# Kernel tuning notes

Hardware: AMD Instinct MI355X
Metric: run time of the kernel (lower is better)

The kernel has to match this reference:

```python
import jax, jax.numpy as jnp
import numpy as np

B, S, V, D, H, KVH, L = 2, 1024, 8192, 1024, 16, 4, 8
HD = D // H          # 64, head dim
KV = KVH * HD        # 256, kv projection width
HID = 2736           # max(16, ceil(2*4*1024/48)*16)
NS = 4               # num_skip_weights = min(L//2, L - L//2)
SOFTCAP = 30.0
ROPE_BASE = 10000.0
RS_INIT = 1.0 / np.sqrt(L)


def setup_inputs() -> dict:
    key = jax.random.key(0)
    ks = iter(jax.random.split(key, 64))
    def rn(shape, s=0.02):
        return jax.random.normal(next(ks), shape, dtype=jnp.float32) * s
    inp = {}
    inp['idx'] = jax.random.randint(next(ks), (B, S), 0, V)
    inp['tok_emb'] = rn((V, D))
    inp['embed_norm_w'] = 1.0 + rn((D,))
    inp['resid_mix'] = jnp.stack([1.0 + rn((L, D), 0.05), rn((L, D), 0.05)], axis=1)  # [L,2,D]
    inp['attn_norm_w'] = 1.0 + rn((L, D))
    inp['mlp_norm_w'] = 1.0 + rn((L, D))
    inp['attn_scale'] = RS_INIT + rn((L, D))
    inp['mlp_scale'] = RS_INIT + rn((L, D))
    inp['Wq'] = rn((L, D, D))
    inp['Wk'] = rn((L, KV, D))
    inp['Wv'] = rn((L, KV, D))
    conv = lambda C: rn((L, 3, C), 0.1).at[:, 2, :].add(1.0)  # curr ~ 1, prev ~ 0
    inp['q_conv_w'] = conv(D)
    inp['k_conv_w'] = conv(KV)
    inp['v_conv_w'] = conv(KV)
    inp['q_gain'] = jnp.eye(H, dtype=jnp.float32)[None] + rn((L, H, H))
    inp['post_attn_norm_w'] = 1.0 + rn((L, D))
    inp['Wo'] = rn((L, D, D))
    inp['Wfc'] = rn((L, HID, D))
    inp['Wgate'] = rn((L, HID, D))
    inp['h_conv_w'] = rn((L, 3, HID), 0.1).at[:, 2, :].add(1.0)
    inp['h_norm_w'] = 1.0 + rn((L, HID))
    inp['Wmproj'] = rn((L, D, HID))
    inp['skip_weights'] = RS_INIT + rn((NS, D))
    inp['skip_gates'] = rn((NS, D), 0.1)
    inp['final_norm_w'] = 1.0 + rn((D,))
    inp['lm_head_w'] = rn((V, D))
    inp['bigram_head'] = rn((V, V))
    inp['bigram_scale'] = 0.02 + rn((V,), 0.005)
    inp['bigram_gate'] = rn((D,), 0.1)
    inp['unigram_bias'] = rn((V,), 0.01)
    return inp


def _rmsnorm(x, w=None):
    eps = jnp.finfo(x.dtype).eps
    y = x * jax.lax.rsqrt(jnp.mean(x * x, axis=-1, keepdims=True) + eps)
    return y * w if w is not None else y


def _dwconv(x, w):  # x [B,S,C], w [3,C]: causal depthwise 3-tap conv
    n = x.shape[1]
    xp = jnp.pad(x, ((0, 0), (2, 0), (0, 0)))
    return w[0] * xp[:, :n] + w[1] * xp[:, 1:n + 1] + w[2] * xp[:, 2:]


def _rope_tables(seqlen):
    inv_freq = 1.0 / (ROPE_BASE ** (jnp.arange(0, HD, 2, dtype=jnp.float32) / HD))
    freqs = jnp.outer(jnp.arange(seqlen, dtype=jnp.float32), inv_freq)  # [S, HD//2]
    return jnp.cos(freqs)[None, None], jnp.sin(freqs)[None, None]


def _apply_rope(x, cos, sin):
    half = x.shape[-1] // 2
    x1, x2 = x[..., :half], x[..., half:]
    return jnp.concatenate([x1 * cos + x2 * sin, -x1 * sin + x2 * cos], axis=-1)


def reference(idx, tok_emb, embed_norm_w, resid_mix, attn_norm_w, mlp_norm_w, attn_scale, mlp_scale, Wq, Wk, Wv, q_conv_w, k_conv_w, v_conv_w, q_gain, post_attn_norm_w, Wo, Wfc, Wgate, h_conv_w, h_norm_w, Wmproj, skip_weights, skip_gates, final_norm_w, lm_head_w, bigram_head, bigram_scale, bigram_gate, unigram_bias):
    cos, sin = _rope_tables(S)
    causal = jnp.tril(jnp.ones((S, S), dtype=bool))

    def attn(x, i):
        q = _dwconv(x @ Wq[i].T, q_conv_w[i]).reshape(B, S, H, HD).transpose(0, 2, 1, 3)
        k = _dwconv(x @ Wk[i].T, k_conv_w[i]).reshape(B, S, KVH, HD).transpose(0, 2, 1, 3)
        v = _dwconv(x @ Wv[i].T, v_conv_w[i]).reshape(B, S, KVH, HD).transpose(0, 2, 1, 3)
        q = _apply_rope(_rmsnorm(q), cos, sin)
        k = _apply_rope(_rmsnorm(k), cos, sin)
        q = jnp.einsum('hg,bgsd->bhsd', q_gain[i], q)
        kr = jnp.repeat(k, H // KVH, axis=1)
        vr = jnp.repeat(v, H // KVH, axis=1)
        scores = jnp.einsum('bhsd,bhtd->bhst', q, kr) / np.sqrt(HD).astype(np.float32)
        scores = jnp.where(causal, scores, -jnp.inf)
        p = jax.nn.softmax(scores, axis=-1)
        y = jnp.einsum('bhst,bhtd->bhsd', p, vr).transpose(0, 2, 1, 3).reshape(B, S, D)
        return _rmsnorm(y, post_attn_norm_w[i]) @ Wo[i].T

    def mlp(x, i):
        h = (x @ Wfc[i].T) * jax.nn.silu(x @ Wgate[i].T)
        h = _rmsnorm(_dwconv(h, h_conv_w[i]), h_norm_w[i])
        return h @ Wmproj[i].T

    def block(x, x0, i):
        x = resid_mix[i, 0] * x + resid_mix[i, 1] * x0
        x = x + attn_scale[i] * attn(_rmsnorm(x, attn_norm_w[i]), i)
        x = x + mlp_scale[i] * mlp(_rmsnorm(x, mlp_norm_w[i]), i)
        return x

    x = _rmsnorm(tok_emb[idx], embed_norm_w)
    x0 = x
    enc = L // 2
    skips = []
    for i in range(enc):
        x = block(x, x0, i)
        skips.append(x)
    for j in range(L - enc):
        if j < NS:
            x = x + (skip_weights[j] * jax.nn.sigmoid(skip_gates[j]))[None, None, :] * skips.pop()
        x = block(x, x0, enc + j)
    x = _rmsnorm(x, final_norm_w)

    logits = x @ lm_head_w.T + unigram_bias
    gate = jax.nn.sigmoid(x @ bigram_gate)[..., None]        # [B,S,1]
    logits = logits + gate * (bigram_head[idx] * bigram_scale)
    return SOFTCAP * jnp.tanh(logits / SOFTCAP)
```

## Files before the change

kernel.cpp:

```cpp
#include <hip/hip_runtime.h>
#include <hip/hip_bf16.h>
#include <cstdint>
#include <cstddef>

#define B_   2
#define S_   1024
#define V_   8192
#define D_   1024
#define H_   16
#define KVH_ 4
#define L_   8
#define HD_  64
#define KV_  256
#define HID_ 2736
#define HIDP 2752
#define NT_  (B_*S_)
#define EPSF 1.1920928955078125e-7f
#define SOFTCAPF 30.0f

typedef __bf16 bf8 __attribute__((ext_vector_type(8)));
typedef __bf16 bf4 __attribute__((ext_vector_type(4)));
typedef float  f4  __attribute__((ext_vector_type(4)));

#define GLDS16(g, l) __builtin_amdgcn_global_load_lds( \
    (const __attribute__((address_space(1))) void*)(g), \
    (__attribute__((address_space(3))) void*)(l), 16, 0, 0)

__device__ __forceinline__ float wsum(float v){
#pragma unroll
  for (int m = 32; m >= 1; m >>= 1) v += __shfl_xor(v, m, 64);
  return v;
}
__device__ __forceinline__ float blocksum256(float v){
  __shared__ float red[4];
  v = wsum(v);
  if ((threadIdx.x & 63) == 0) red[threadIdx.x >> 6] = v;
  __syncthreads();
  return red[0] + red[1] + red[2] + red[3];
}
__device__ __forceinline__ float4 ld4b(const __bf16* p, size_t i4){
  bf4 v = ((const bf4*)p)[i4];
  return make_float4((float)v[0], (float)v[1], (float)v[2], (float)v[3]);
}

template<int BM, int BN, int OUT>
__global__ __launch_bounds__(256) void k_gemm(
    const __bf16* __restrict__ A, const __bf16* __restrict__ Wt,
    void* __restrict__ Cv, int M, int N, int K, int lda, int mtiles,
    const int* __restrict__ idx, const float* __restrict__ gateb,
    const float* __restrict__ bhd, const float* __restrict__ bsc,
    const float* __restrict__ ub)
{
  constexpr int SMEM = ((BM + BN) * 128 > 32768 || OUT == 2) ? 32768 : (BM + BN) * 128;
  __shared__ __attribute__((aligned(16))) unsigned char smem[SMEM];
  __bf16* As = (__bf16*)smem;
  __bf16* Bs = (__bf16*)(smem + BM*128);

  const int tid  = threadIdx.x;
  const int nwg = gridDim.x;
  const int wg  = (blockIdx.x & 7) * (nwg >> 3) + (blockIdx.x >> 3);
  const int bm   = wg % mtiles;
  const int bn   = wg / mtiles;
  const int m0   = bm * BM, n0 = bn * BN;
  const int lane = tid & 63, wv = tid >> 6;
  const int wm   = (wv >> 1) * (BM / 2);
  const int wn   = (wv & 1) * (BN / 2);
  const int fr   = lane & 15, g = lane >> 4;
  constexpr int MI = BM / 32;
  constexpr int NJ = BN / 32;
  constexpr int AP = BM / 32;
  constexpr int BP = BN / 32;

  f4 acc[MI][NJ] = {};

  const int rs = lane >> 3, ss = lane & 7;
  const int cseg = ss ^ ((wv*8 + rs) & 7);
  const __bf16* aq[AP];
#pragma unroll
  for (int p = 0; p < AP; ++p)
    aq[p] = A + (size_t)(m0 + wv*8 + p*32 + rs) * lda + cseg*8;
  const __bf16* bq[BP];
#pragma unroll
  for (int p = 0; p < BP; ++p) {
    int rB = n0 + wv*8 + p*32 + rs; if (rB > N-1) rB = N-1;
    bq[p] = Wt + (size_t)rB * K + cseg*8;
  }

  for (int k0 = 0; k0 < K; k0 += 64) {
    __syncthreads();
#pragma unroll
    for (int p = 0; p < AP; ++p) GLDS16(aq[p] + k0, As + (wv*8 + p*32)*64);
#pragma unroll
    for (int p = 0; p < BP; ++p) GLDS16(bq[p] + k0, Bs + (wv*8 + p*32)*64);
    __syncthreads();

#pragma unroll
    for (int ks = 0; ks < 2; ++ks) {
      const int sgo = (((ks*4 + g) ^ (fr & 7)) << 3);
      bf8 af[MI], bf[NJ];
#pragma unroll
      for (int i = 0; i < MI; ++i)
        af[i] = *(const bf8*)&As[(wm + i*16 + fr)*64 + sgo];
#pragma unroll
      for (int j = 0; j < NJ; ++j)
        bf[j] = *(const bf8*)&Bs[(wn + j*16 + fr)*64 + sgo];
#pragma unroll
      for (int i = 0; i < MI; ++i)
#pragma unroll
        for (int j = 0; j < NJ; ++j)
          acc[i][j] = __builtin_amdgcn_mfma_f32_16x16x32_bf16(af[i], bf[j], acc[i][j], 0, 0, 0);
    }
  }

  if constexpr (OUT == 2) {
    float* EP = (float*)smem;
    __syncthreads();
#pragma unroll
    for (int i = 0; i < MI; ++i)
#pragma unroll
      for (int j = 0; j < NJ; ++j)
#pragma unroll
        for (int r = 0; r < 4; ++r)
          EP[(wm + i*16 + g*4 + r)*128 + wn + j*16 + fr] = acc[i][j][r];
    __syncthreads();
#pragma unroll
    for (int it = 0; it < 8; ++it) {
      int row = it*8 + (tid >> 5);
      int c0  = (tid & 31) << 2;
      int grow = m0 + row;
      int gn   = n0 + c0;
      float gt = gateb[grow];
      int   tk = idx[grow];
      float4 a4 = *(float4*)&EP[row*128 + c0];
      float4 b4 = *(const float4*)&bhd[(size_t)tk * V_ + gn];
      float4 u4 = *(const float4*)&ub[gn];
      float4 s4 = *(const float4*)&bsc[gn];
      float4 o;
      o.x = SOFTCAPF * tanhf((a4.x + u4.x + gt*b4.x*s4.x) / SOFTCAPF);
      o.y = SOFTCAPF * tanhf((a4.y + u4.y + gt*b4.y*s4.y) / SOFTCAPF);
      o.z = SOFTCAPF * tanhf((a4.z + u4.z + gt*b4.z*s4.z) / SOFTCAPF);
      o.w = SOFTCAPF * tanhf((a4.w + u4.w + gt*b4.w*s4.w) / SOFTCAPF);
      *(float4*)&((float*)Cv)[(size_t)grow * N + gn] = o;
    }
  } else {
    const int rbase = g << 2;
#pragma unroll
    for (int i = 0; i < MI; ++i) {
      int gm = m0 + wm + i*16 + rbase;
#pragma unroll
      for (int j = 0; j < NJ; ++j) {
        int gn = n0 + wn + j*16 + fr;
        if (gn < N) {
          if constexpr (OUT == 1) {
#pragma unroll
            for (int r = 0; r < 4; ++r)
              ((__bf16*)Cv)[(size_t)(gm + r) * N + gn] = (__bf16)acc[i][j][r];
          } else {
#pragma unroll
            for (int r = 0; r < 4; ++r)
              ((float*)Cv)[(size_t)(gm + r) * N + gn] = acc[i][j][r];
          }
        }
      }
    }
  }
}

__global__ void k_cvt(const float* __restrict__ s, __bf16* __restrict__ d,
                      int perL, int K, int Kpad, long dstL, long dstOff, long nd4)
{
  long i = (long)blockIdx.x * 256 + threadIdx.x;
  if (i >= nd4) return;
  const int kp4 = Kpad >> 2;
  long row = i / kp4;
  int  c   = (int)(i % kp4) << 2;
  long layer = row / perL, r = row % perL;
  bf4 o;
  if (c < K) {
    float4 v = *(const float4*)(s + (layer*perL + r) * (long)K + c);
    o[0] = (__bf16)v.x; o[1] = (__bf16)v.y; o[2] = (__bf16)v.z; o[3] = (__bf16)v.w;
  } else { o[0] = o[1] = o[2] = o[3] = (__bf16)0.f; }
  *(bf4*)(d + layer*dstL + dstOff + (long)r*Kpad + c) = o;
}

__global__ void k_embed(const int* __restrict__ idx, const float* __restrict__ emb,
                        const float* __restrict__ wn, float* __restrict__ x, float* __restrict__ x0)
{
  const int r = blockIdx.x, t = threadIdx.x;
  const float4 v = ((const float4*)(emb + (size_t)idx[r] * D_))[t];
  float ss = blocksum256(v.x*v.x + v.y*v.y + v.z*v.z + v.w*v.w);
  float rs = rsqrtf(ss / (float)D_ + EPSF);
  const float4 w = ((const float4*)wn)[t];
  float4 o = make_float4(v.x*rs*w.x, v.y*rs*w.y, v.z*rs*w.z, v.w*rs*w.w);
  ((float4*)(x  + (size_t)r * D_))[t] = o;
  ((float4*)(x0 + (size_t)r * D_))[t] = o;
}

__global__ void k_blockstart(
    float* __restrict__ x, const float* __restrict__ x0,
    const __bf16* __restrict__ t1, const float* __restrict__ msc,
    float* __restrict__ skstore, const float* __restrict__ skread, int same,
    const float* __restrict__ skw, const float* __restrict__ skg,
    const float* __restrict__ mix, const float* __restrict__ nw,
    __bf16* __restrict__ xn)
{
  const int r = blockIdx.x, t = threadIdx.x;
  const size_t i4 = (size_t)r * 256 + t;
  float4 xv = ((float4*)x)[i4];
  if (t1) {
    float4 tv = ld4b(t1, i4);
    float4 s  = ((const float4*)msc)[t];
    xv.x += s.x*tv.x; xv.y += s.y*tv.y; xv.z += s.z*tv.z; xv.w += s.w*tv.w;
  }
  if (skstore) ((float4*)skstore)[i4] = xv;
  if (skw) {
    float4 sv;
    if (same) sv = xv;
    else      sv = ((const float4*)skread)[i4];
    float4 w = ((const float4*)skw)[t];
// ... 65 lines not shown
  float bb = (s >= 1) ? (float)p0[-ld]   : 0.f;
  return w[c]*a + w[C + c]*bb + w[2*C + c]*(float)p0[0];
}

__global__ __launch_bounds__(256) void k_prep(
    const __bf16* __restrict__ qkv,
    const float* __restrict__ qcw, const float* __restrict__ kcw, const float* __restrict__ vcw,
    const float* __restrict__ qgain,
    __bf16* __restrict__ q2, __bf16* __restrict__ k2, __bf16* __restrict__ v2)
{
  const int tok = blockIdx.x;
  const int s = tok & (S_ - 1);
  const int t = threadIdx.x, lane = t & 63, w = t >> 6;
  __shared__ float qsh[1024];

  const int j = lane & 31;
  float freq = __expf(-(float)j * (9.210340371976184f / 32.f));
  float sn, cs;
  __sincosf((float)s * freq, &sn, &cs);

#pragma unroll
  for (int k = 0; k < 4; ++k) {
    int c = t + k*256;
    float qc = conv3b(qkv, tok, s, 1536, c, qcw, D_, c);
    float ssq = wsum(qc * qc);
    float qn = qc * rsqrtf(ssq / 64.f + EPSF);
    float pr = __shfl_xor(qn, 32, 64);
    qsh[c] = qn * cs + ((lane < 32) ? pr * sn : -pr * sn);
  }
  __syncthreads();
  float qg[16];
#pragma unroll
  for (int g = 0; g < 16; ++g) qg[g] = qsh[g*64 + lane];
#pragma unroll
  for (int k = 0; k < 4; ++k) {
    int h = (k << 2) + w;
    float acc = 0.f;
#pragma unroll
    for (int g = 0; g < 16; ++g) acc += qgain[h*16 + g] * qg[g];
    q2[(size_t)tok * D_ + h*64 + lane] = (__bf16)acc;
  }

  {
    float kc = conv3b(qkv, tok, s, 1536, 1024 + t, kcw, KV_, t);
    float ssk = wsum(kc * kc);
    float kn = kc * rsqrtf(ssk / 64.f + EPSF);
    float pk = __shfl_xor(kn, 32, 64);
    k2[(size_t)tok * KV_ + t] = (__bf16)(kn * cs + ((lane < 32) ? pk * sn : -pk * sn));
  }
  v2[(size_t)tok * KV_ + t] = (__bf16)conv3b(qkv, tok, s, 1536, 1280 + t, vcw, KV_, t);
}

#define LDK 72
__global__ __launch_bounds__(256) void k_attn(
    const __bf16* __restrict__ q2, const __bf16* __restrict__ k2,
    const __bf16* __restrict__ v2, float* __restrict__ y)
{
  __shared__ __attribute__((aligned(16))) __bf16 Ks[64*LDK];
  __shared__ __attribute__((aligned(16))) __bf16 Vt[64*LDK];
  __shared__ __attribute__((aligned(16))) __bf16 Ps[4][16*LDK];

  const int id = blockIdx.x;
  const int qb = id & 15;
  const int h  = (id >> 4) & 15;
  const int b  = id >> 8;
  const int tid = threadIdx.x, l = tid & 63, wq = tid >> 6;
  const int g = l >> 4, fr = l & 15;
  const int kvh = h >> 2;
  const int qrow = qb*64 + wq*16 + fr;

  bf8 qf[2];
#pragma unroll
  for (int ks = 0; ks < 2; ++ks)
    qf[ks] = *(const bf8*)&q2[(size_t)(b*S_ + qrow)*D_ + h*64 + g*8 + ks*32];

  float m = -1e30f, lsum = 0.f;
  f4 acc[4] = {};

  const int nch = qb + 1;
  for (int ch = 0; ch < nch; ++ch) {
    const int t0 = ch << 6;
    __syncthreads();
#pragma unroll
    for (int it = 0; it < 2; ++it) {
      int i = tid + it*256;
      int row = i >> 3, seg = (i & 7) << 3;
      *(bf8*)&Ks[row*LDK + seg] =
        *(const bf8*)&k2[(size_t)(b*S_ + t0 + row)*KV_ + kvh*64 + seg];
    }
    {
      int key4 = (tid & 15) << 2, hd4 = (tid >> 4) << 2;
      bf4 vv[4];
#pragma unroll
      for (int kk = 0; kk < 4; ++kk)
        vv[kk] = *(const bf4*)&v2[(size_t)(b*S_ + t0 + key4 + kk)*KV_ + kvh*64 + hd4];
#pragma unroll
      for (int hh = 0; hh < 4; ++hh) {
        bf4 w = { vv[0][hh], vv[1][hh], vv[2][hh], vv[3][hh] };
        *(bf4*)&Vt[(hd4 + hh)*LDK + key4] = w;
      }
    }
    __syncthreads();

    f4 sc[4] = {};
#pragma unroll
    for (int ks = 0; ks < 2; ++ks)
#pragma unroll
      for (int t = 0; t < 4; ++t) {
        bf8 kf = *(const bf8*)&Ks[(t*16 + fr)*LDK + g*8 + ks*32];
        sc[t] = __builtin_amdgcn_mfma_f32_16x16x32_bf16(kf, qf[ks], sc[t], 0, 0, 0);
      }

    const bool lastch = (ch == qb);
    float s[4][4];
    float pmax = -1e30f;
#pragma unroll
    for (int t = 0; t < 4; ++t)
#pragma unroll
      for (int r = 0; r < 4; ++r) {
        float v = sc[t][r] * 0.125f;
        if (lastch && (t0 + t*16 + g*4 + r > qrow)) v = -1e30f;
        s[t][r] = v;
        pmax = fmaxf(pmax, v);
      }
    pmax = fmaxf(pmax, __shfl_xor(pmax, 16, 64));
    pmax = fmaxf(pmax, __shfl_xor(pmax, 32, 64));
    float mnew = fmaxf(m, pmax);
    float alpha = __expf(m - mnew);
    float rs = 0.f;
#pragma unroll
    for (int t = 0; t < 4; ++t)
#pragma unroll
      for (int r = 0; r < 4; ++r) { float p = __expf(s[t][r] - mnew); s[t][r] = p; rs += p; }
    rs += __shfl_xor(rs, 16, 64);
    rs += __shfl_xor(rs, 32, 64);
    lsum = lsum * alpha + rs;
    m = mnew;
#pragma unroll
    for (int t = 0; t < 4; ++t) acc[t] = acc[t] * alpha;

#pragma unroll
    for (int t = 0; t < 4; ++t) {
      bf4 pw = { (__bf16)s[t][0], (__bf16)s[t][1], (__bf16)s[t][2], (__bf16)s[t][3] };
      *(bf4*)&Ps[wq][fr*LDK + t*16 + g*4] = pw;
    }

#pragma unroll
    for (int ks = 0; ks < 2; ++ks) {
      bf8 pf = *(const bf8*)&Ps[wq][fr*LDK + g*8 + ks*32];
#pragma unroll
      for (int t = 0; t < 4; ++t) {
        bf8 vf = *(const bf8*)&Vt[(t*16 + fr)*LDK + g*8 + ks*32];
        acc[t] = __builtin_amdgcn_mfma_f32_16x16x32_bf16(vf, pf, acc[t], 0, 0, 0);
      }
    }
  }

  float inv = 1.f / lsum;
#pragma unroll
  for (int t = 0; t < 4; ++t)
#pragma unroll
    for (int r = 0; r < 4; ++r)
      y[(size_t)(b*S_ + qrow)*D_ + h*64 + t*16 + g*4 + r] = acc[t][r] * inv;
}

__device__ __forceinline__ float hprodb(const __bf16* row, int c){
  float a = (float)row[c], b = (float)row[HID_ + c];
  return a * b / (1.f + __expf(-b));
}
__global__ __launch_bounds__(256) void k_hfuse(
    const __bf16* __restrict__ hb, const float* __restrict__ cw,
    const float* __restrict__ nw, __bf16* __restrict__ out)
{
  const int tok = blockIdx.x, t = threadIdx.x;
  const int s = tok & (S_ - 1);
  const __bf16* row0 = hb + (size_t)tok * 5472;
  float v[11]; float ss = 0.f;
#pragma unroll
  for (int ii = 0; ii < 11; ++ii) {
    int c = t + ii*256;
    float cv = 0.f;
    if (c < HID_) {
      float p0 = hprodb(row0, c);
      float p1 = (s >= 1) ? hprodb(row0 - 5472, c) : 0.f;
      float p2 = (s >= 2) ? hprodb(row0 - 2*5472, c) : 0.f;
      cv = cw[c]*p2 + cw[HID_ + c]*p1 + cw[2*HID_ + c]*p0;
    }
    v[ii] = cv; ss += cv*cv;
  }
  ss = blocksum256(ss);
  float rs = rsqrtf(ss / (float)HID_ + EPSF);
#pragma unroll
  for (int ii = 0; ii < 11; ++ii) {
    int c = t + ii*256;
    if (c < HIDP)
      out[(size_t)tok * HIDP + c] = (c < HID_) ? (__bf16)(v[ii]*rs*nw[c]) : (__bf16)0.f;
  }
}

template<int BM, int BN, int OUT>
static inline void gemm(const __bf16* A, const __bf16* W, void* C, int M, int N, int K,
                        int lda, hipStream_t s,
                        const int* idx = nullptr, const float* gateb = nullptr,
                        const float* bhd = nullptr, const float* bsc = nullptr,
                        const float* ub = nullptr)
{
  int mt = M / BM, nt = (N + BN - 1) / BN;
  k_gemm<BM, BN, OUT><<<dim3(mt * nt), dim3(256), 0, s>>>(A, W, C, M, N, K, lda, mt,
                                                          idx, gateb, bhd, bsc, ub);
}

extern "C" void kernel_launch(void* const* d_in, const int* in_sizes, int n_in,
                              void* d_out, int out_size, void* d_ws, size_t ws_size,
                              hipStream_t stream)
{
  const int*   idx    = (const int*)d_in[0];
  const float* temb   = (const float*)d_in[1];
  const float* enw    = (const float*)d_in[2];
  const float* rmix   = (const float*)d_in[3];
  const float* anw    = (const float*)d_in[4];
  const float* mnw    = (const float*)d_in[5];
  const float* ascale = (const float*)d_in[6];
  const float* mscale = (const float*)d_in[7];
  const float* Wq     = (const float*)d_in[8];
  const float* Wk     = (const float*)d_in[9];
  const float* Wv     = (const float*)d_in[10];
  const float* qcw    = (const float*)d_in[11];
  const float* kcw    = (const float*)d_in[12];
  const float* vcw    = (const float*)d_in[13];
  const float* qgain  = (const float*)d_in[14];
  const float* panw   = (const float*)d_in[15];
  const float* Wo     = (const float*)d_in[16];
  const float* Wfc    = (const float*)d_in[17];
  const float* Wgate  = (const float*)d_in[18];
  const float* hcw    = (const float*)d_in[19];
  const float* hnw    = (const float*)d_in[20];
  const float* Wmp    = (const float*)d_in[21];
  const float* skw    = (const float*)d_in[22];
  const float* skg    = (const float*)d_in[23];
  const float* fnw    = (const float*)d_in[24];
  const float* lmw    = (const float*)d_in[25];
  const float* bh     = (const float*)d_in[26];
  const float* bsc    = (const float*)d_in[27];
  const float* bg     = (const float*)d_in[28];
  const float* ub     = (const float*)d_in[29];

  float* p = (float*)d_ws;
  float* x    = p; p += (size_t)NT_ * D_;
  float* x0   = p; p += (size_t)NT_ * D_;
  float* y    = p; p += (size_t)NT_ * D_;
  float* skips= p; p += (size_t)4 * NT_ * D_;
  float* gateb= p; p += NT_;
  __bf16* qkvb= (__bf16*)p; p += (size_t)NT_ * 1536 / 2;
  __bf16* hbb = (__bf16*)p; p += (size_t)NT_ * 5472 / 2;
  __bf16* t1b = (__bf16*)p; p += (size_t)NT_ * D_ / 2;
  __bf16* xnb = (__bf16*)p; p += (size_t)NT_ * D_ / 2;
  __bf16* q2b = (__bf16*)p; p += (size_t)NT_ * D_ / 2;
  __bf16* k2b = (__bf16*)p; p += (size_t)NT_ * KV_ / 2;
  __bf16* v2b = (__bf16*)p; p += (size_t)NT_ * KV_ / 2;
  __bf16* hnb = (__bf16*)p; p += (size_t)NT_ * HIDP / 2;
  __bf16* wqkv= (__bf16*)p; p += (size_t)L_ * 1536 * 1024 / 2;
  __bf16* wob = (__bf16*)p; p += (size_t)L_ * 1024 * 1024 / 2;
  __bf16* wfcg= (__bf16*)p; p += (size_t)L_ * 5472 * 1024 / 2;
  __bf16* wmpb= (__bf16*)p; p += (size_t)L_ * 1024 * HIDP / 2;
  __bf16* wlmb= (__bf16*)p; p += (size_t)V_ * 1024 / 2;
  float* logits = (float*)d_out;

  auto cvt = [&](const float* s, __bf16* d, int perL, int K, int Kpad,
                 long dstL, long dstOff, int nl) {
    long nd4 = (long)nl * perL * (Kpad >> 2);
    int grid = (int)((nd4 + 255) / 256);
    k_cvt<<<grid, 256, 0, stream>>>(s, d, perL, K, Kpad, dstL, dstOff, nd4);
  };
  cvt(Wq,    wqkv, 1024, 1024, 1024, 1536L*1024, 0,          L_);
  cvt(Wk,    wqkv,  256, 1024, 1024, 1536L*1024, 1024L*1024, L_);
  cvt(Wv,    wqkv,  256, 1024, 1024, 1536L*1024, 1280L*1024, L_);
  cvt(Wo,    wob,  1024, 1024, 1024, 1024L*1024, 0,          L_);
  cvt(Wfc,   wfcg, 2736, 1024, 1024, 5472L*1024, 0,          L_);
  cvt(Wgate, wfcg, 2736, 1024, 1024, 5472L*1024, 2736L*1024, L_);
  cvt(Wmp,   wmpb, 1024, 2736, HIDP, 1024L*HIDP, 0,          L_);
  cvt(lmw,   wlmb, 8192, 1024, 1024, 8192L*1024, 0,          1);

  k_embed<<<NT_, 256, 0, stream>>>(idx, temb, enw, x, x0);

  for (int i = 0; i < L_; ++i) {
    const float* pmsc = (i > 0) ? mscale + (size_t)(i-1) * D_ : nullptr;
    float* skst = (i >= 1 && i <= 4) ? skips + (size_t)(i-1) * NT_ * D_ : nullptr;
    const float* skrd = (i >= 4) ? skips + (size_t)(7-i) * NT_ * D_ : nullptr;
    const float* swp = (i >= 4) ? skw + (size_t)(i-4) * D_ : nullptr;
    const float* sgp = (i >= 4) ? skg + (size_t)(i-4) * D_ : nullptr;
    k_blockstart<<<NT_, 256, 0, stream>>>(x, x0, (i > 0) ? t1b : nullptr, pmsc,
                                          skst, skrd, (i == 4) ? 1 : 0, swp, sgp,
                                          rmix + (size_t)i * 2 * D_,
                                          anw + (size_t)i * D_, xnb);
    gemm<64, 128, 1>(xnb, wqkv + (size_t)i * 1536 * 1024, qkvb, NT_, 1536, 1024, 1024, stream);
    k_prep<<<NT_, 256, 0, stream>>>(qkvb,
                                    qcw + (size_t)i * 3 * D_, kcw + (size_t)i * 3 * KV_,
                                    vcw + (size_t)i * 3 * KV_, qgain + (size_t)i * H_ * H_,
                                    q2b, k2b, v2b);
    k_attn<<<B_ * H_ * (S_/64), 256, 0, stream>>>(q2b, k2b, v2b, y);
    k_rmsnormb<<<NT_, 256, 0, stream>>>(y, panw + (size_t)i * D_, xnb);
    gemm<64, 64, 1>(xnb, wob + (size_t)i * 1024 * 1024, t1b, NT_, 1024, 1024, 1024, stream);
    k_addnorm<<<NT_, 256, 0, stream>>>(x, t1b, ascale + (size_t)i * D_,
                                       mnw + (size_t)i * D_, xnb, nullptr, nullptr);
    gemm<64, 128, 1>(xnb, wfcg + (size_t)i * 5472 * 1024, hbb, NT_, 5472, 1024, 1024, stream);
    k_hfuse<<<NT_, 256, 0, stream>>>(hbb, hcw + (size_t)i * 3 * HID_,
                                     hnw + (size_t)i * HID_, hnb);
    gemm<64, 64, 1>(hnb, wmpb + (size_t)i * 1024 * HIDP, t1b, NT_, 1024, HIDP, HIDP, stream);
  }

  k_addnorm<<<NT_, 256, 0, stream>>>(x, t1b, mscale + (size_t)7 * D_, fnw, xnb, bg, gateb);
  gemm<64, 128, 2>(xnb, wlmb, logits, NT_, V_, 1024, 1024, stream, idx, gateb, bh, bsc, ub);
}
```

Baseline: 1.920 ms.

## Add 256x256 triple-buffered 8-wave GEMM for MLP up-projection and LM head

Adds a new GEMM kernel with 256x256 tiles, 512 threads (8 waves), three LDS buffers fed by global_load_lds, explicit vmcnt waits and barriers, and setprio around the MFMA bursts. It is used for the large fc/gate projection (N=5472) and the LM head with its fused bigram/softcap epilogue, which now runs in four 64-row passes through LDS. The goal is more operand reuse per loaded byte and overlap of loads with MFMA. The cost is 96KB of LDS per block, which limits occupancy, and wasted work on partial N tiles, since 5472 is not a multiple of 256 and out-of-range B rows are clamped.

New measurement: 1.914 ms. Within noise of the previous version (-0.3%).

```diff
diff --git a/kernel.cpp b/kernel.cpp
--- a/kernel.cpp
+++ b/kernel.cpp
@@ -46,12 +46,9 @@
 template<int BM, int BN, int OUT>
 __global__ __launch_bounds__(256) void k_gemm(
     const __bf16* __restrict__ A, const __bf16* __restrict__ Wt,
-    void* __restrict__ Cv, int M, int N, int K, int lda, int mtiles,
-    const int* __restrict__ idx, const float* __restrict__ gateb,
-    const float* __restrict__ bhd, const float* __restrict__ bsc,
-    const float* __restrict__ ub)
-{
-  constexpr int SMEM = ((BM + BN) * 128 > 32768 || OUT == 2) ? 32768 : (BM + BN) * 128;
+    void* __restrict__ Cv, int M, int N, int K, int lda, int mtiles)
+{
+  constexpr int SMEM = (BM + BN) * 128;
   __shared__ __attribute__((aligned(16))) unsigned char smem[SMEM];
   __bf16* As = (__bf16*)smem;
   __bf16* Bs = (__bf16*)(smem + BM*128);
@@ -112,59 +109,181 @@
     }
   }
 
-  if constexpr (OUT == 2) {
+  const int rbase = g << 2;
+#pragma unroll
+  for (int i = 0; i < MI; ++i) {
+    int gm = m0 + wm + i*16 + rbase;
+#pragma unroll
+    for (int j = 0; j < NJ; ++j) {
+      int gn = n0 + wn + j*16 + fr;
+      if (gn < N) {
+        if constexpr (OUT == 1) {
+#pragma unroll
+          for (int r = 0; r < 4; ++r)
+            ((__bf16*)Cv)[(size_t)(gm + r) * N + gn] = (__bf16)acc[i][j][r];
+        } else {
+#pragma unroll
+          for (int r = 0; r < 4; ++r)
+            ((float*)Cv)[(size_t)(gm + r) * N + gn] = acc[i][j][r];
+        }
+      }
+    }
+  }
+}
+
+#define STG8(t, h, b) do { \
+    if ((h) < 2) { \
+      const __bf16* _s = A + (size_t)(m0 + (h)*128 + w16 + rsub) * lda + (t)*32 + sseg*8; \
+      GLDS16(_s, smem + (b)*32768 + ((h)*128 + w16) * 64); \
+    } else { \
+      int _rB = n0 + ((h)-2)*128 + w16 + rsub; if (_rB > N-1) _rB = N-1; \
+      const __bf16* _s = Wt + (size_t)_rB * K + (t)*32 + sseg*8; \
+      GLDS16(_s, smem + (b)*32768 + 16384 + (((h)-2)*128 + w16) * 64); \
+    } } while (0)
+
+#define LDA8(b, r, gg) (*(const bf8*)(smem + (b)*32768 + (r)*64 + (((gg) ^ ((((r)>>3)&1)<<1)))*16))
+#define LDB8(b, r, gg) (*(const bf8*)(smem + (b)*32768 + 16384 + (r)*64 + (((gg) ^ ((((r)>>3)&1)<<1)))*16))
+
+#define PH8(bt, q, dostage, st, sh, sb, W) do { \
+    const int _r0 = wr*128 + ((q)>>1)*64 + fr; \
+    const int _c0 = wc*64 + ((q)&1)*32 + fr; \
+    bf8 _a0 = LDA8(bt, _r0 +  0, g); \
+    bf8 _a1 = LDA8(bt, _r0 + 16, g); \
+    bf8 _a2 = LDA8(bt, _r0 + 32, g); \
+    bf8 _a3 = LDA8(bt, _r0 + 48, g); \
+    bf8 _b0 = LDB8(bt, _c0 +  0, g); \
+    bf8 _b1 = LDB8(bt, _c0 + 16, g); \
+    if (dostage) STG8(st, sh, sb); \
+    if ((W) == 4)      asm volatile("s_waitcnt vmcnt(4)" ::: "memory"); \
+    else if ((W) == 0) asm volatile("s_waitcnt vmcnt(0)" ::: "memory"); \
+    asm volatile("" ::: "memory"); \
+    __builtin_amdgcn_s_barrier(); \
+    asm volatile("" ::: "memory"); \
+    __builtin_amdgcn_s_setprio(1); \
+    acc[((q)>>1)*4+0][((q)&1)*2+0] = __builtin_amdgcn_mfma_f32_16x16x32_bf16(_a0, _b0, acc[((q)>>1)*4+0][((q)&1)*2+0], 0,0,0); \
+    acc[((q)>>1)*4+0][((q)&1)*2+1] = __builtin_amdgcn_mfma_f32_16x16x32_bf16(_a0, _b1, acc[((q)>>1)*4+0][((q)&1)*2+1], 0,0,0); \
+    acc[((q)>>1)*4+1][((q)&1)*2+0] = __builtin_amdgcn_mfma_f32_16x16x32_bf16(_a1, _b0, acc[((q)>>1)*4+1][((q)&1)*2+0], 0,0,0); \
+    acc[((q)>>1)*4+1][((q)&1)*2+1] = __builtin_amdgcn_mfma_f32_16x16x32_bf16(_a1, _b1, acc[((q)>>1)*4+1][((q)&1)*2+1], 0,0,0); \
+    acc[((q)>>1)*4+2][((q)&1)*2+0] = __builtin_amdgcn_mfma_f32_16x16x32_bf16(_a2, _b0, acc[((q)>>1)*4+2][((q)&1)*2+0], 0,0,0); \
+    acc[((q)>>1)*4+2][((q)&1)*2+1] = __builtin_amdgcn_mfma_f32_16x16x32_bf16(_a2, _b1, acc[((q)>>1)*4+2][((q)&1)*2+1], 0,0,0); \
+    acc[((q)>>1)*4+3][((q)&1)*2+0] = __builtin_amdgcn_mfma_f32_16x16x32_bf16(_a3, _b0, acc[((q)>>1)*4+3][((q)&1)*2+0], 0,0,0); \
+    acc[((q)>>1)*4+3][((q)&1)*2+1] = __builtin_amdgcn_mfma_f32_16x16x32_bf16(_a3, _b1, acc[((q)>>1)*4+3][((q)&1)*2+1], 0,0,0); \
+    __builtin_amdgcn_s_setprio(0); \
+    asm volatile("" ::: "memory"); \
+    __builtin_amdgcn_s_barrier(); \
+    asm volatile("" ::: "memory"); \
+  } while (0)
+
+template<int OUT>
+__global__ __launch_bounds__(512, 2) void k_gemm8(
+    const __bf16* __restrict__ A, const __bf16* __restrict__ Wt,
+    void* __restrict__ Cv, int M, int N, int K, int lda, int mtiles,
+    const int* __restrict__ idx, const float* __restrict__ gateb,
+    const float* __restrict__ bhd, const float* __restrict__ bsc,
+    const float* __restrict__ ub)
+{
+  __shared__ __attribute__((aligned(16))) unsigned char smem[98304];
+  const int tid = threadIdx.x;
+  const int nwg = gridDim.x;
+  const int wg  = (blockIdx.x & 7) * (nwg >> 3) + (blockIdx.x >> 3);
+  const int bm = wg % mtiles, bnn = wg / mtiles;
+  const int m0 = bm << 8, n0 = bnn << 8;
+  const int l = tid & 63, wid = tid >> 6;
+  const int wr = wid >> 2, wc = wid & 3;
+  const int fr = l & 15, g = l >> 4;
+
+  f4 acc[8][4] = {};
+
+  const int w16  = wid * 16;
+  const int rsub = l >> 2;
+  const int sseg = (l & 3) ^ ((l >= 32) ? 2 : 0);
+
+  const int nk = K >> 5;
+  const int ni = nk >> 1;
+
+  STG8(0, 0, 0); STG8(0, 1, 0); STG8(0, 2, 0); STG8(0, 3, 0);
+  STG8(1, 0, 1); STG8(1, 1, 1); STG8(1, 2, 1); STG8(1, 3, 1);
+  asm volatile("s_waitcnt vmcnt(4)" ::: "memory");
+  asm volatile("" ::: "memory");
+  __builtin_amdgcn_s_barrier();
+  asm volatile("" ::: "memory");
+
+  int b0 = 0;
+  for (int i = 0; i < ni; ++i) {
+    const int b1 = (b0 == 2) ? 0 : b0 + 1;
+    const int b2 = (b1 == 2) ? 0 : b1 + 1;
+    const bool nlast = (i + 1 < ni);
+    const int t2 = 2*i + 2, t3 = 2*i + 3;
+    PH8(b0, 0, nlast, t2, 0, b2, -1);
+    PH8(b0, 1, nlast, t2, 1, b2, -1);
+    PH8(b0, 2, nlast, t2, 2, b2, -1);
+    PH8(b0, 3, nlast, t2, 3, b2, nlast ? 4 : 0);
+    PH8(b1, 0, nlast, t3, 0, b0, -1);
+    PH8(b1, 1, nlast, t3, 1, b0, -1);
+    PH8(b1, 2, nlast, t3, 2, b0, -1);
+    PH8(b1, 3, nlast, t3, 3, b0, nlast ? 4 : -1);
+    b0 = b2;
+  }
+
+  if constexpr (OUT == 1) {
+    __bf16* C = (__bf16*)Cv;
+#pragma unroll
+    for (int ii = 0; ii < 8; ++ii) {
+      int gm = m0 + wr*128 + ii*16 + g*4;
+#pragma unroll
+      for (int j = 0; j < 4; ++j) {
+        int gn = n0 + wc*64 + j*16 + fr;
+        if (gn < N) {
+#pragma unroll
+          for (int r = 0; r < 4; ++r)
+            C[(size_t)(gm + r) * N + gn] = (__bf16)acc[ii][j][r];
+        }
+      }
+    }
+  } else {
     float* EP = (float*)smem;
     __syncthreads();
 #pragma unroll
-    for (int i = 0; i < MI; ++i)
-#pragma unroll
-      for (int j = 0; j < NJ; ++j)
-#pragma unroll
-        for (int r = 0; r < 4; ++r)
-          EP[(wm + i*16 + g*4 + r)*128 + wn + j*16 + fr] = acc[i][j][r];
-    __syncthreads();
-#pragma unroll
-    for (int it = 0; it < 8; ++it) {
-      int row = it*8 + (tid >> 5);
-      int c0  = (tid & 31) << 2;
-      int grow = m0 + row;
-      int gn   = n0 + c0;
-      float gt = gateb[grow];
-      int   tk = idx[grow];
-      float4 a4 = *(float4*)&EP[row*128 + c0];
-      float4 b4 = *(const float4*)&bhd[(size_t)tk * V_ + gn];
-      float4 u4 = *(const float4*)&ub[gn];
-      float4 s4 = *(const float4*)&bsc[gn];
-      float4 o;
-      o.x = SOFTCAPF * tanhf((a4.x + u4.x + gt*b4.x*s4.x) / SOFTCAPF);
-      o.y = SOFTCAPF * tanhf((a4.y + u4.y + gt*b4.y*s4.y) / SOFTCAPF);
-      o.z = SOFTCAPF * tanhf((a4.z + u4.z + gt*b4.z*s4.z) / SOFTCAPF);
-      o.w = SOFTCAPF * tanhf((a4.w + u4.w + gt*b4.w*s4.w) / SOFTCAPF);
-      *(float4*)&((float*)Cv)[(size_t)grow * N + gn] = o;
-    }
-  } else {
-    const int rbase = g << 2;
-#pragma unroll
-    for (int i = 0; i < MI; ++i) {
-      int gm = m0 + wm + i*16 + rbase;
-#pragma unroll
-      for (int j = 0; j < NJ; ++j) {
-        int gn = n0 + wn + j*16 + fr;
-        if (gn < N) {
-          if constexpr (OUT == 1) {
+    for (int pass = 0; pass < 4; ++pass) {
+      if (wr == (pass >> 1)) {
+#pragma unroll
+        for (int a = 0; a < 4; ++a) {
+          int ii = (pass & 1)*4 + a;
+#pragma unroll
+          for (int j = 0; j < 4; ++j)
 #pragma unroll
             for (int r = 0; r < 4; ++r)
-              ((__bf16*)Cv)[(size_t)(gm + r) * N + gn] = (__bf16)acc[i][j][r];
-          } else {
-#pragma unroll
-            for (int r = 0; r < 4; ++r)
-              ((float*)Cv)[(size_t)(gm + r) * N + gn] = acc[i][j][r];
-          }
+              EP[(a*16 + g*4 + r)*256 + wc*64 + j*16 + fr] = acc[ii][j][r];
         }
       }
-    }
-  }
-}
+      __syncthreads();
+#pragma unroll
+      for (int it = 0; it < 8; ++it) {
+        int row = it*8 + (tid >> 6);
+        int c0  = (tid & 63) << 2;
+        int grow = m0 + pass*64 + row;
+        int gn = n0 + c0;
+        float gt = gateb[grow];
+        int tk = idx[grow];
+        float4 a4 = *(float4*)&EP[row*256 + c0];
+        float4 b4 = *(const float4*)&bhd[(size_t)tk * V_ + gn];
+        float4 u4 = *(const float4*)&ub[gn];
+        float4 s4 = *(const float4*)&bsc[gn];
+        float4 o;
+        o.x = SOFTCAPF * tanhf((a4.x + u4.x + gt*b4.x*s4.x) / SOFTCAPF);
+        o.y = SOFTCAPF * tanhf((a4.y + u4.y + gt*b4.y*s4.y) / SOFTCAPF);
+        o.z = SOFTCAPF * tanhf((a4.z + u4.z + gt*b4.z*s4.z) / SOFTCAPF);
+        o.w = SOFTCAPF * tanhf((a4.w + u4.w + gt*b4.w*s4.w) / SOFTCAPF);
+        *(float4*)&((float*)Cv)[(size_t)grow * N + gn] = o;
+      }
+      __syncthreads();
+    }
+  }
+}
+#undef PH8
+#undef LDA8
+#undef LDB8
+#undef STG8
 
 __global__ void k_cvt(const float* __restrict__ s, __bf16* __restrict__ d,
                       int perL, int K, int Kpad, long dstL, long dstOff, long nd4)
@@ -484,14 +603,22 @@
 
 template<int BM, int BN, int OUT>
 static inline void gemm(const __bf16* A, const __bf16* W, void* C, int M, int N, int K,
-                        int lda, hipStream_t s,
-                        const int* idx = nullptr, const float* gateb = nullptr,
-                        const float* bhd = nullptr, const float* bsc = nullptr,
-                        const float* ub = nullptr)
+                        int lda, hipStream_t s)
 {
   int mt = M / BM, nt = (N + BN - 1) / BN;
-  k_gemm<BM, BN, OUT><<<dim3(mt * nt), dim3(256), 0, s>>>(A, W, C, M, N, K, lda, mt,
-                                                          idx, gateb, bhd, bsc, ub);
+  k_gemm<BM, BN, OUT><<<dim3(mt * nt), dim3(256), 0, s>>>(A, W, C, M, N, K, lda, mt);
+}
+
+template<int OUT>
+static inline void gemm8(const __bf16* A, const __bf16* W, void* C, int M, int N, int K,
+                         int lda, hipStream_t s,
+                         const int* idx = nullptr, const float* gateb = nullptr,
+                         const float* bhd = nullptr, const float* bsc = nullptr,
+                         const float* ub = nullptr)
+{
+  int mt = M >> 8, nt = (N + 255) >> 8;
+  k_gemm8<OUT><<<dim3(mt * nt), dim3(512), 0, s>>>(A, W, C, M, N, K, lda, mt,
+                                                   idx, gateb, bhd, bsc, ub);
 }
 
 extern "C" void kernel_launch(void* const* d_in, const int* in_sizes, int n_in,
@@ -587,12 +714,12 @@
     gemm<64, 64, 1>(xnb, wob + (size_t)i * 1024 * 1024, t1b, NT_, 1024, 1024, 1024, stream);
     k_addnorm<<<NT_, 256, 0, stream>>>(x, t1b, ascale + (size_t)i * D_,
                                        mnw + (size_t)i * D_, xnb, nullptr, nullptr);
-    gemm<64, 128, 1>(xnb, wfcg + (size_t)i * 5472 * 1024, hbb, NT_, 5472, 1024, 1024, stream);
+    gemm8<1>(xnb, wfcg + (size_t)i * 5472 * 1024, hbb, NT_, 5472, 1024, 1024, stream);
     k_hfuse<<<NT_, 256, 0, stream>>>(hbb, hcw + (size_t)i * 3 * HID_,
                                      hnw + (size_t)i * HID_, hnb);
     gemm<64, 64, 1>(hnb, wmpb + (size_t)i * 1024 * HIDP, t1b, NT_, 1024, HIDP, HIDP, stream);
   }
 
   k_addnorm<<<NT_, 256, 0, stream>>>(x, t1b, mscale + (size_t)7 * D_, fnw, xnb, bg, gateb);
-  gemm<64, 128, 2>(xnb, wlmb, logits, NT_, V_, 1024, 1024, stream, idx, gateb, bh, bsc, ub);
-}
+  gemm8<2>(xnb, wlmb, logits, NT_, V_, 1024, 1024, stream, idx, gateb, bh, bsc, ub);
+}
```

## Replace LDS-staged GEMM with register-direct 128x128 tiles; widen attention key chunks

Applied to the files above, without the earlier changes.

The GEMM kernel drops LDS staging and barriers and instead loads MFMA fragments directly from global memory into double-buffered registers, computing 128x128 output tiles per block. The logits epilogue is split into two passes through a smaller shared buffer. The attention kernel processes 128 keys per chunk instead of 64, halving loop iterations and barriers. The trade-off is loss of shared-memory reuse across waves and strided global fragment loads in the GEMM, plus more masked work on the diagonal in attention.

New measurement: 2.938 ms. 53.0% more time.

```diff
diff --git a/kernel.cpp b/kernel.cpp
--- a/kernel.cpp
+++ b/kernel.cpp
@@ -22,10 +22,6 @@
 typedef __bf16 bf4 __attribute__((ext_vector_type(4)));
 typedef float  f4  __attribute__((ext_vector_type(4)));
 
-#define GLDS16(g, l) __builtin_amdgcn_global_load_lds( \
-    (const __attribute__((address_space(1))) void*)(g), \
-    (__attribute__((address_space(3))) void*)(l), 16, 0, 0)
-
 __device__ __forceinline__ float wsum(float v){
 #pragma unroll
   for (int m = 32; m >= 1; m >>= 1) v += __shfl_xor(v, m, 64);
@@ -43,123 +39,115 @@
   return make_float4((float)v[0], (float)v[1], (float)v[2], (float)v[3]);
 }
 
-template<int BM, int BN, int OUT>
-__global__ __launch_bounds__(256) void k_gemm(
+template<int OUT>
+__global__ __launch_bounds__(256) void k_gemmr(
     const __bf16* __restrict__ A, const __bf16* __restrict__ Wt,
     void* __restrict__ Cv, int M, int N, int K, int lda, int mtiles,
     const int* __restrict__ idx, const float* __restrict__ gateb,
     const float* __restrict__ bhd, const float* __restrict__ bsc,
     const float* __restrict__ ub)
 {
-  constexpr int SMEM = ((BM + BN) * 128 > 32768 || OUT == 2) ? 32768 : (BM + BN) * 128;
-  __shared__ __attribute__((aligned(16))) unsigned char smem[SMEM];
-  __bf16* As = (__bf16*)smem;
-  __bf16* Bs = (__bf16*)(smem + BM*128);
-
-  const int tid  = threadIdx.x;
+  __shared__ __attribute__((aligned(16))) float EP[(OUT == 2) ? 64*128 : 4];
+
+  const int tid = threadIdx.x;
   const int nwg = gridDim.x;
   const int wg  = (blockIdx.x & 7) * (nwg >> 3) + (blockIdx.x >> 3);
-  const int bm   = wg % mtiles;
-  const int bn   = wg / mtiles;
-  const int m0   = bm * BM, n0 = bn * BN;
-  const int lane = tid & 63, wv = tid >> 6;
-  const int wm   = (wv >> 1) * (BM / 2);
-  const int wn   = (wv & 1) * (BN / 2);
-  const int fr   = lane & 15, g = lane >> 4;
-  constexpr int MI = BM / 32;
-  constexpr int NJ = BN / 32;
-  constexpr int AP = BM / 32;
-  constexpr int BP = BN / 32;
-
-  f4 acc[MI][NJ] = {};
-
-  const int rs = lane >> 3, ss = lane & 7;
-  const int cseg = ss ^ ((wv*8 + rs) & 7);
-  const __bf16* aq[AP];
-#pragma unroll
-  for (int p = 0; p < AP; ++p)
-    aq[p] = A + (size_t)(m0 + wv*8 + p*32 + rs) * lda + cseg*8;
-  const __bf16* bq[BP];
-#pragma unroll
-  for (int p = 0; p < BP; ++p) {
-    int rB = n0 + wv*8 + p*32 + rs; if (rB > N-1) rB = N-1;
-    bq[p] = Wt + (size_t)rB * K + cseg*8;
-  }
-
-  for (int k0 = 0; k0 < K; k0 += 64) {
-    __syncthreads();
-#pragma unroll
-    for (int p = 0; p < AP; ++p) GLDS16(aq[p] + k0, As + (wv*8 + p*32)*64);
-#pragma unroll
-    for (int p = 0; p < BP; ++p) GLDS16(bq[p] + k0, Bs + (wv*8 + p*32)*64);
-    __syncthreads();
-
-#pragma unroll
-    for (int ks = 0; ks < 2; ++ks) {
-      const int sgo = (((ks*4 + g) ^ (fr & 7)) << 3);
-      bf8 af[MI], bf[NJ];
-#pragma unroll
-      for (int i = 0; i < MI; ++i)
-        af[i] = *(const bf8*)&As[(wm + i*16 + fr)*64 + sgo];
-#pragma unroll
-      for (int j = 0; j < NJ; ++j)
-        bf[j] = *(const bf8*)&Bs[(wn + j*16 + fr)*64 + sgo];
-#pragma unroll
-      for (int i = 0; i < MI; ++i)
-#pragma unroll
-        for (int j = 0; j < NJ; ++j)
-          acc[i][j] = __builtin_amdgcn_mfma_f32_16x16x32_bf16(af[i], bf[j], acc[i][j], 0, 0, 0);
-    }
-  }
+  const int bm  = wg % mtiles, bn = wg / mtiles;
+  const int m0  = bm << 7, n0 = bn << 7;
+  const int l = tid & 63, wv = tid >> 6;
+  const int wr = (wv >> 1) << 6;
+  const int wc = (wv & 1) << 6;
+  const int fr = l & 15, g = l >> 4;
+
+  f4 acc[4][4] = {};
+
+  const __bf16* ap[4];
+  const __bf16* bp[4];
+#pragma unroll
+  for (int i = 0; i < 4; ++i)
+    ap[i] = A + (size_t)(m0 + wr + i*16 + fr) * lda + g*8;
+#pragma unroll
+  for (int j = 0; j < 4; ++j) {
+    int rB = n0 + wc + j*16 + fr; if (rB > N-1) rB = N-1;
+    bp[j] = Wt + (size_t)rB * K + g*8;
+  }
+
+#define MFMA16(AF, BF) do { \
+    _Pragma("unroll") \
+    for (int i = 0; i < 4; ++i) \
+      _Pragma("unroll") \
+      for (int j = 0; j < 4; ++j) \
+        acc[i][j] = __builtin_amdgcn_mfma_f32_16x16x32_bf16(AF[i], BF[j], acc[i][j], 0, 0, 0); \
+  } while (0)
+
+  bf8 a0[4], b0[4], a1[4], b1[4];
+#pragma unroll
+  for (int i = 0; i < 4; ++i) { a0[i] = *(const bf8*)(ap[i]); b0[i] = *(const bf8*)(bp[i]); }
+
+  for (int k0 = 0; k0 + 64 <= K; k0 += 64) {
+#pragma unroll
+    for (int i = 0; i < 4; ++i) {
+      a1[i] = *(const bf8*)(ap[i] + k0 + 32);
+      b1[i] = *(const bf8*)(bp[i] + k0 + 32);
+    }
+    MFMA16(a0, b0);
+    if (k0 + 64 < K) {
+#pragma unroll
+      for (int i = 0; i < 4; ++i) {
+        a0[i] = *(const bf8*)(ap[i] + k0 + 64);
+        b0[i] = *(const bf8*)(bp[i] + k0 + 64);
+      }
+    }
+    MFMA16(a1, b1);
+  }
+#undef MFMA16
 
   if constexpr (OUT == 2) {
-    float* EP = (float*)smem;
-    __syncthreads();
-#pragma unroll
-    for (int i = 0; i < MI; ++i)
-#pragma unroll
-      for (int j = 0; j < NJ; ++j)
-#pragma unroll
-        for (int r = 0; r < 4; ++r)
-          EP[(wm + i*16 + g*4 + r)*128 + wn + j*16 + fr] = acc[i][j][r];
-    __syncthreads();
-#pragma unroll
-    for (int it = 0; it < 8; ++it) {
-      int row = it*8 + (tid >> 5);
-      int c0  = (tid & 31) << 2;
-      int grow = m0 + row;
-      int gn   = n0 + c0;
-      float gt = gateb[grow];
-      int   tk = idx[grow];
-      float4 a4 = *(float4*)&EP[row*128 + c0];
-      float4 b4 = *(const float4*)&bhd[(size_t)tk * V_ + gn];
-      float4 u4 = *(const float4*)&ub[gn];
-      float4 s4 = *(const float4*)&bsc[gn];
-      float4 o;
-      o.x = SOFTCAPF * tanhf((a4.x + u4.x + gt*b4.x*s4.x) / SOFTCAPF);
-      o.y = SOFTCAPF * tanhf((a4.y + u4.y + gt*b4.y*s4.y) / SOFTCAPF);
-      o.z = SOFTCAPF * tanhf((a4.z + u4.z + gt*b4.z*s4.z) / SOFTCAPF);
-      o.w = SOFTCAPF * tanhf((a4.w + u4.w + gt*b4.w*s4.w) / SOFTCAPF);
-      *(float4*)&((float*)Cv)[(size_t)grow * N + gn] = o;
+#pragma unroll
+    for (int pass = 0; pass < 2; ++pass) {
+      __syncthreads();
+      if ((wv >> 1) == pass) {
+#pragma unroll
+        for (int i = 0; i < 4; ++i)
+#pragma unroll
+          for (int j = 0; j < 4; ++j)
+#pragma unroll
+            for (int r = 0; r < 4; ++r)
+              EP[(i*16 + g*4 + r)*128 + wc + j*16 + fr] = acc[i][j][r];
+      }
+      __syncthreads();
+#pragma unroll
+      for (int it = 0; it < 8; ++it) {
+        int row = it*8 + (tid >> 5);
+        int c0  = (tid & 31) << 2;
+        int grow = m0 + pass*64 + row;
+        int gn   = n0 + c0;
+        float gt = gateb[grow];
+        int   tk = idx[grow];
+        float4 a4 = *(float4*)&EP[row*128 + c0];
+        float4 b4 = *(const float4*)&bhd[(size_t)tk * V_ + gn];
+        float4 u4 = *(const float4*)&ub[gn];
+        float4 s4 = *(const float4*)&bsc[gn];
+        float4 o;
+        o.x = SOFTCAPF * tanhf((a4.x + u4.x + gt*b4.x*s4.x) / SOFTCAPF);
+        o.y = SOFTCAPF * tanhf((a4.y + u4.y + gt*b4.y*s4.y) / SOFTCAPF);
+        o.z = SOFTCAPF * tanhf((a4.z + u4.z + gt*b4.z*s4.z) / SOFTCAPF);
+        o.w = SOFTCAPF * tanhf((a4.w + u4.w + gt*b4.w*s4.w) / SOFTCAPF);
+        *(float4*)&((float*)Cv)[(size_t)grow * N + gn] = o;
+      }
     }
   } else {
     const int rbase = g << 2;
 #pragma unroll
-    for (int i = 0; i < MI; ++i) {
-      int gm = m0 + wm + i*16 + rbase;
-#pragma unroll
-      for (int j = 0; j < NJ; ++j) {
-        int gn = n0 + wn + j*16 + fr;
+    for (int i = 0; i < 4; ++i) {
+      int gm = m0 + wr + i*16 + rbase;
+#pragma unroll
+      for (int j = 0; j < 4; ++j) {
+        int gn = n0 + wc + j*16 + fr;
         if (gn < N) {
-          if constexpr (OUT == 1) {
-#pragma unroll
-            for (int r = 0; r < 4; ++r)
-              ((__bf16*)Cv)[(size_t)(gm + r) * N + gn] = (__bf16)acc[i][j][r];
-          } else {
-#pragma unroll
-            for (int r = 0; r < 4; ++r)
-              ((float*)Cv)[(size_t)(gm + r) * N + gn] = acc[i][j][r];
-          }
+#pragma unroll
+          for (int r = 0; r < 4; ++r)
+            ((__bf16*)Cv)[(size_t)(gm + r) * N + gn] = (__bf16)acc[i][j][r];
         }
       }
     }
@@ -336,13 +324,14 @@
 }
 
 #define LDK 72
+#define LDP 136
 __global__ __launch_bounds__(256) void k_attn(
     const __bf16* __restrict__ q2, const __bf16* __restrict__ k2,
     const __bf16* __restrict__ v2, float* __restrict__ y)
 {
-  __shared__ __attribute__((aligned(16))) __bf16 Ks[64*LDK];
-  __shared__ __attribute__((aligned(16))) __bf16 Vt[64*LDK];
-  __shared__ __attribute__((aligned(16))) __bf16 Ps[4][16*LDK];
+  __shared__ __attribute__((aligned(16))) __bf16 Ks[128*LDK];
+  __shared__ __attribute__((aligned(16))) __bf16 Vt[64*LDP];
+  __shared__ __attribute__((aligned(16))) __bf16 Ps[4][16*LDP];
 
   const int id = blockIdx.x;
   const int qb = id & 15;
@@ -361,45 +350,45 @@
   float m = -1e30f, lsum = 0.f;
   f4 acc[4] = {};
 
-  const int nch = qb + 1;
+  const int nch = (qb >> 1) + 1;
   for (int ch = 0; ch < nch; ++ch) {
-    const int t0 = ch << 6;
+    const int t0 = ch << 7;
     __syncthreads();
 #pragma unroll
-    for (int it = 0; it < 2; ++it) {
+    for (int it = 0; it < 4; ++it) {
       int i = tid + it*256;
       int row = i >> 3, seg = (i & 7) << 3;
       *(bf8*)&Ks[row*LDK + seg] =
         *(const bf8*)&k2[(size_t)(b*S_ + t0 + row)*KV_ + kvh*64 + seg];
     }
     {
-      int key4 = (tid & 15) << 2, hd4 = (tid >> 4) << 2;
-      bf4 vv[4];
+      int key4 = (tid & 31) << 2, hd8 = (tid >> 5) << 3;
+      bf8 vv[4];
 #pragma unroll
       for (int kk = 0; kk < 4; ++kk)
-        vv[kk] = *(const bf4*)&v2[(size_t)(b*S_ + t0 + key4 + kk)*KV_ + kvh*64 + hd4];
-#pragma unroll
-      for (int hh = 0; hh < 4; ++hh) {
+        vv[kk] = *(const bf8*)&v2[(size_t)(b*S_ + t0 + key4 + kk)*KV_ + kvh*64 + hd8];
+#pragma unroll
+      for (int hh = 0; hh < 8; ++hh) {
         bf4 w = { vv[0][hh], vv[1][hh], vv[2][hh], vv[3][hh] };
-        *(bf4*)&Vt[(hd4 + hh)*LDK + key4] = w;
+        *(bf4*)&Vt[(hd8 + hh)*LDP + key4] = w;
       }
     }
     __syncthreads();
 
-    f4 sc[4] = {};
+    f4 sc[8] = {};
 #pragma unroll
     for (int ks = 0; ks < 2; ++ks)
 #pragma unroll
-      for (int t = 0; t < 4; ++t) {
+      for (int t = 0; t < 8; ++t) {
         bf8 kf = *(const bf8*)&Ks[(t*16 + fr)*LDK + g*8 + ks*32];
         sc[t] = __builtin_amdgcn_mfma_f32_16x16x32_bf16(kf, qf[ks], sc[t], 0, 0, 0);
       }
 
-    const bool lastch = (ch == qb);
-    float s[4][4];
+    const bool lastch = (ch == nch - 1);
+    float s[8][4];
     float pmax = -1e30f;
 #pragma unroll
-    for (int t = 0; t < 4; ++t)
+    for (int t = 0; t < 8; ++t)
 #pragma unroll
       for (int r = 0; r < 4; ++r) {
         float v = sc[t][r] * 0.125f;
@@ -413,7 +402,7 @@
     float alpha = __expf(m - mnew);
     float rs = 0.f;
 #pragma unroll
-    for (int t = 0; t < 4; ++t)
+    for (int t = 0; t < 8; ++t)
 #pragma unroll
       for (int r = 0; r < 4; ++r) { float p = __expf(s[t][r] - mnew); s[t][r] = p; rs += p; }
     rs += __shfl_xor(rs, 16, 64);
@@ -424,17 +413,17 @@
     for (int t = 0; t < 4; ++t) acc[t] = acc[t] * alpha;
 
 #pragma unroll
-    for (int t = 0; t < 4; ++t) {
+    for (int t = 0; t < 8; ++t) {
       bf4 pw = { (__bf16)s[t][0], (__bf16)s[t][1], (__bf16)s[t][2], (__bf16)s[t][3] };
-      *(bf4*)&Ps[wq][fr*LDK + t*16 + g*4] = pw;
-    }
-
-#pragma unroll
-    for (int ks = 0; ks < 2; ++ks) {
-      bf8 pf = *(const bf8*)&Ps[wq][fr*LDK + g*8 + ks*32];
+      *(bf4*)&Ps[wq][fr*LDP + t*16 + g*4] = pw;
+    }
+
+#pragma unroll
+    for (int ks = 0; ks < 4; ++ks) {
+      bf8 pf = *(const bf8*)&Ps[wq][fr*LDP + g*8 + ks*32];
 #pragma unroll
       for (int t = 0; t < 4; ++t) {
-        bf8 vf = *(const bf8*)&Vt[(t*16 + fr)*LDK + g*8 + ks*32];
+        bf8 vf = *(const bf8*)&Vt[(t*16 + fr)*LDP + g*8 + ks*32];
         acc[t] = __builtin_amdgcn_mfma_f32_16x16x32_bf16(vf, pf, acc[t], 0, 0, 0);
       }
     }
@@ -482,16 +471,16 @@
   }
 }
 
-template<int BM, int BN, int OUT>
-static inline void gemm(const __bf16* A, const __bf16* W, void* C, int M, int N, int K,
-                        int lda, hipStream_t s,
-                        const int* idx = nullptr, const float* gateb = nullptr,
-                        const float* bhd = nullptr, const float* bsc = nullptr,
-                        const float* ub = nullptr)
-{
-  int mt = M / BM, nt = (N + BN - 1) / BN;
-  k_gemm<BM, BN, OUT><<<dim3(mt * nt), dim3(256), 0, s>>>(A, W, C, M, N, K, lda, mt,
-                                                          idx, gateb, bhd, bsc, ub);
+template<int OUT>
+static inline void gemmr(const __bf16* A, const __bf16* W, void* C, int M, int N, int K,
+                         int lda, hipStream_t s,
+                         const int* idx = nullptr, const float* gateb = nullptr,
+                         const float* bhd = nullptr, const float* bsc = nullptr,
+                         const float* ub = nullptr)
+{
+  int mt = M >> 7, nt = (N + 127) >> 7;
+  k_gemmr<OUT><<<dim3(mt * nt), dim3(256), 0, s>>>(A, W, C, M, N, K, lda, mt,
+                                                   idx, gateb, bhd, bsc, ub);
 }
 
 extern "C" void kernel_launch(void* const* d_in, const int* in_sizes, int n_in,
@@ -577,22 +566,22 @@
                                           skst, skrd, (i == 4) ? 1 : 0, swp, sgp,
                                           rmix + (size_t)i * 2 * D_,
                                           anw + (size_t)i * D_, xnb);
-    gemm<64, 128, 1>(xnb, wqkv + (size_t)i * 1536 * 1024, qkvb, NT_, 1536, 1024, 1024, stream);
+    gemmr<1>(xnb, wqkv + (size_t)i * 1536 * 1024, qkvb, NT_, 1536, 1024, 1024, stream);
     k_prep<<<NT_, 256, 0, stream>>>(qkvb,
                                     qcw + (size_t)i * 3 * D_, kcw + (size_t)i * 3 * KV_,
                                     vcw + (size_t)i * 3 * KV_, qgain + (size_t)i * H_ * H_,
                                     q2b, k2b, v2b);
     k_attn<<<B_ * H_ * (S_/64), 256, 0, stream>>>(q2b, k2b, v2b, y);
     k_rmsnormb<<<NT_, 256, 0, stream>>>(y, panw + (size_t)i * D_, xnb);
-    gemm<64, 64, 1>(xnb, wob + (size_t)i * 1024 * 1024, t1b, NT_, 1024, 1024, 1024, stream);
+    gemmr<1>(xnb, wob + (size_t)i * 1024 * 1024, t1b, NT_, 1024, 1024, 1024, stream);
     k_addnorm<<<NT_, 256, 0, stream>>>(x, t1b, ascale + (size_t)i * D_,
                                        mnw + (size_t)i * D_, xnb, nullptr, nullptr);
-    gemm<64, 128, 1>(xnb, wfcg + (size_t)i * 5472 * 1024, hbb, NT_, 5472, 1024, 1024, stream);
+    gemmr<1>(xnb, wfcg + (size_t)i * 5472 * 1024, hbb, NT_, 5472, 1024, 1024, stream);
     k_hfuse<<<NT_, 256, 0, stream>>>(hbb, hcw + (size_t)i * 3 * HID_,
                                      hnw + (size_t)i * HID_, hnb);
-    gemm<64, 64, 1>(hnb, wmpb + (size_t)i * 1024 * HIDP, t1b, NT_, 1024, HIDP, HIDP, stream);
+    gemmr<1>(hnb, wmpb + (size_t)i * 1024 * HIDP, t1b, NT_, 1024, HIDP, HIDP, stream);
   }
 
   k_addnorm<<<NT_, 256, 0, stream>>>(x, t1b, mscale + (size_t)7 * D_, fnw, xnb, bg, gateb);
-  gemm<64, 128, 2>(xnb, wlmb, logits, NT_, V_, 1024, 1024, stream, idx, gateb, bh, bsc, ub);
-}
+  gemmr<2>(xnb, wlmb, logits, NT_, V_, 1024, 1024, stream, idx, gateb, bh, bsc, ub);
+}
```
